# Kernel optimization log

Measured on AMD Instinct MI355X. Metric: run time of the kernel, lower is better.

The kernel has to match this reference:

```python
import jax, jax.numpy as jnp
import numpy as np

N, H = 8192, 256
TOP_K = 16          # k = min(top_k, N-1)
TEMPERATURE = 1.0
NEG_SLOPE = 0.2
NUM_SECTORS = 11


def setup_inputs() -> dict:
    key = jax.random.key(0)
    kE, kW, ka, ks, kA = jax.random.split(key, 5)
    embeddings = jax.random.normal(kE, (N, H), dtype=jnp.float32)
    # xavier-uniform-like scale for W (nn.Linear, bias=False)
    lim = float(np.sqrt(6.0 / (H + H)))
    W = jax.random.uniform(kW, (H, H), dtype=jnp.float32, minval=-lim, maxval=lim)
    # a ~ Normal(0, 1/sqrt(2H))
    a = jax.random.normal(ka, (2 * H,), dtype=jnp.float32) * (1.0 / np.sqrt(2 * H))
    sector_ids = jax.random.randint(ks, (N,), 0, NUM_SECTORS, dtype=jnp.int32)
    active_mask = jax.random.randint(kA, (N,), 0, 2, dtype=jnp.int32).astype(bool)
    return {"embeddings": embeddings, "W": W, "a": a,
            "sector_ids": sector_ids, "active_mask": active_mask}


def reference(embeddings, W, a, sector_ids, active_mask):
    # h = W(embeddings)  (torch Linear: x @ W.T)
    h = embeddings @ W.T                                   # [N, H]
    # attention[i,j] = leaky_relu(a . [h_i, h_j]) = leaky_relu(a1.h_i + a2.h_j)
    # (decomposition of the concat+matmul; same math, avoids O(N^2*2H) tensor)
    a1, a2 = a[:H], a[H:]
    s_i = h @ a1                                           # [N]
    s_j = h @ a2                                           # [N]
    att = jax.nn.leaky_relu(s_i[:, None] + s_j[None, :], NEG_SLOPE) / TEMPERATURE
    # combined mask: active pairs AND same sector
    mask = (active_mask[:, None] & active_mask[None, :]) \
           & (sector_ids[:, None] == sector_ids[None, :])  # [N, N]
    att = jnp.where(mask, att, -jnp.inf)
    k = min(TOP_K, N - 1)
    topk_values, topk_indices = jax.lax.top_k(att, k)      # [N, k] each
    valid = jnp.isfinite(topk_values)                      # invalid = masked-out slots
    # dense padded representation of (edge_index, edge_weight):
    # src = topk_indices, dst = row index, weight = topk_values where valid
    edge_weight = jnp.where(valid, topk_values, 0.0)
    return edge_weight, topk_indices, valid
```

## Files before the change

kernel.cpp:

```cpp
#include <hip/hip_runtime.h>

#define N 8192
#define H 256
#define TOPK 16
#define NSEC 11
#define NEG_SLOPE 0.2
#define NB 256
#define NT 256
#define RPB (N / NB)
#define NSL 8
#define SLICE (N / NSL)
#define NWB 256
#define IDX_SENT 0x7fffffff

__device__ __forceinline__ bool better(double av, int ai, double bv, int bi) {
    return (av > bv) || (av == bv && ai < bi);
}

__global__ __launch_bounds__(NT) void compute_v_s(
    const float* __restrict__ E, const float* __restrict__ W,
    const float* __restrict__ a,
    float* __restrict__ s1f, double* __restrict__ s2g,
    int* __restrict__ arrive)
{
    __shared__ float sa[2 * H];
    __shared__ double sv1[H];
    __shared__ double sv2[H];

    int t = threadIdx.x;
    int blk = blockIdx.x;
    int lane = t & 63;
    int w = t >> 6;

    if (blk == 0 && t <= NSEC) arrive[t] = 0;

    sa[t] = a[t];
    sa[t + H] = a[t + H];
    __syncthreads();

    {
        double a1_0 = 0.0, a1_1 = 0.0, a1_2 = 0.0, a1_3 = 0.0;
        double a2_0 = 0.0, a2_1 = 0.0, a2_2 = 0.0, a2_3 = 0.0;
        for (int j = 0; j < H; j += 4) {
            double w0 = (double)W[(j + 0) * H + t];
            double w1 = (double)W[(j + 1) * H + t];
            double w2 = (double)W[(j + 2) * H + t];
            double w3 = (double)W[(j + 3) * H + t];
            a1_0 += w0 * (double)sa[j + 0];
            a1_1 += w1 * (double)sa[j + 1];
            a1_2 += w2 * (double)sa[j + 2];
            a1_3 += w3 * (double)sa[j + 3];
            a2_0 += w0 * (double)sa[H + j + 0];
            a2_1 += w1 * (double)sa[H + j + 1];
            a2_2 += w2 * (double)sa[H + j + 2];
            a2_3 += w3 * (double)sa[H + j + 3];
        }
        sv1[t] = (a1_0 + a1_1) + (a1_2 + a1_3);
        sv2[t] = (a2_0 + a2_1) + (a2_2 + a2_3);
    }
    __syncthreads();

    {
        float4 e[RPB / 4];
#pragma unroll
        for (int q = 0; q < RPB / 4; ++q) {
            int row = blk * RPB + (w + 4 * q);
            e[q] = ((const float4*)(E + (size_t)row * H))[lane];
        }
        int base = lane * 4;
        double b10 = sv1[base + 0], b11 = sv1[base + 1],
               b12 = sv1[base + 2], b13 = sv1[base + 3];
        double b20 = sv2[base + 0], b21 = sv2[base + 1],
               b22 = sv2[base + 2], b23 = sv2[base + 3];
#pragma unroll
        for (int q = 0; q < RPB / 4; ++q) {
            int row = blk * RPB + (w + 4 * q);
            double acc1 = (double)e[q].x * b10 + (double)e[q].y * b11 +
                          (double)e[q].z * b12 + (double)e[q].w * b13;
            double acc2 = (double)e[q].x * b20 + (double)e[q].y * b21 +
                          (double)e[q].z * b22 + (double)e[q].w * b23;
            for (int o = 32; o > 0; o >>= 1) {
                acc1 += __shfl_down(acc1, o);
                acc2 += __shfl_down(acc2, o);
            }
            if (lane == 0) {
                s1f[row] = (float)acc1;
                s2g[row] = acc2;
            }
        }
    }
}

__global__ __launch_bounds__(NT) void slice_merge_write(
    const float* __restrict__ s1f, const double* __restrict__ s2g,
    const int* __restrict__ sec, const int* __restrict__ act,
    double* __restrict__ candV, int* __restrict__ candI,
    int* __restrict__ cnts, int* __restrict__ arrive,
    int* __restrict__ top_idx, int* __restrict__ fill_idx,
    int* __restrict__ m_arr, float* __restrict__ out)
{
    __shared__ double wV[4][TOPK];
    __shared__ int wI[4][TOPK];
    __shared__ int wCnt[4];
    __shared__ int sLast;

    int bx = blockIdx.x;
    int t = threadIdx.x;
    int lane = t & 63;
    int w = t >> 6;
    int* done = arrive + NSEC;

    if (bx < NSEC * NSL) {
        int c = bx >> 3;
        int sl = bx & 7;

        int j0 = sl * SLICE + 4 * t;
        int4 a4 = *(const int4*)(act + j0);
        int4 s4 = *(const int4*)(sec + j0);
        double2 d01 = *(const double2*)(s2g + j0);
        double2 d23 = *(const double2*)(s2g + j0 + 2);

        bool p0 = (a4.x != 0) && (s4.x == c);
        bool p1 = (a4.y != 0) && (s4.y == c);
        bool p2 = (a4.z != 0) && (s4.z == c);
        bool p3 = (a4.w != 0) && (s4.w == c);

        double v[4];
        int ix[4];
        v[0] = p0 ? d01.x : -INFINITY;  ix[0] = p0 ? (j0 + 0) : IDX_SENT;
        v[1] = p1 ? d01.y : -INFINITY;  ix[1] = p1 ? (j0 + 1) : IDX_SENT;
        v[2] = p2 ? d23.x : -INFINITY;  ix[2] = p2 ? (j0 + 2) : IDX_SENT;
        v[3] = p3 ? d23.y : -INFINITY;  ix[3] = p3 ? (j0 + 3) : IDX_SENT;

        int cnt = __popcll(__ballot(p0)) + __popcll(__ballot(p1)) +
                  __popcll(__ballot(p2)) + __popcll(__ballot(p3));

        for (int r = 0; r < TOPK; ++r) {
            double bv = v[0];
            int bi = ix[0];
#pragma unroll
            for (int p = 1; p < 4; ++p)
                if (better(v[p], ix[p], bv, bi)) { bv = v[p]; bi = ix[p]; }
            for (int o = 32; o > 0; o >>= 1) {
                double ov = __shfl_xor(bv, o);
                int oi = __shfl_xor(bi, o);
                if (better(ov, oi, bv, bi)) { bv = ov; bi = oi; }
            }
#pragma unroll
            for (int p = 0; p < 4; ++p)
                if (ix[p] == bi) { v[p] = -INFINITY; ix[p] = IDX_SENT; }
            if (lane == 0) {
                wV[w][r] = bv;
                wI[w][r] = bi;
            }
        }
        if (lane == 0) wCnt[w] = cnt;
        __syncthreads();

        if (w == 0) {
            double mv = wV[lane >> 4][lane & 15];
            int mi = wI[lane >> 4][lane & 15];
            for (int r = 0; r < TOPK; ++r) {
                double bv = mv;
                int bi = mi;
                for (int o = 32; o > 0; o >>= 1) {
                    double ov = __shfl_xor(bv, o);
                    int oi = __shfl_xor(bi, o);
                    if (better(ov, oi, bv, bi)) { bv = ov; bi = oi; }
                }
                if (mi == bi) { mv = -INFINITY; mi = IDX_SENT; }
                if (lane == 0) {
                    candV[bx * TOPK + r] = bv;
                    candI[bx * TOPK + r] = bi;
                }
            }
            if (lane == 0) {
                cnts[bx] = wCnt[0] + wCnt[1] + wCnt[2] + wCnt[3];
                __threadfence();
                int old = atomicAdd(&arrive[c], 1);
                sLast = (old == NSL - 1);
            }
        }
        __syncthreads();

        if (sLast) {
            __threadfence();

            if (w == 0) {
                const double* cbV = candV + (size_t)c * NSL * TOPK;
                const int* cbI = candI + (size_t)c * NSL * TOPK;
                double v0 = cbV[lane];
                int i0 = cbI[lane];
                double v1 = cbV[lane + 64];
                int i1 = cbI[lane + 64];
                for (int r = 0; r < TOPK; ++r) {
                    double bv;
                    int bi;
                    if (better(v0, i0, v1, i1)) { bv = v0; bi = i0; }
                    else                        { bv = v1; bi = i1; }
                    for (int o = 32; o > 0; o >>= 1) {
                        double ov = __shfl_xor(bv, o);
                        int oi = __shfl_xor(bi, o);
                        if (better(ov, oi, bv, bi)) { bv = ov; bi = oi; }
                    }
                    if (i0 == bi)      { v0 = -INFINITY; i0 = IDX_SENT; }
                    else if (i1 == bi) { v1 = -INFINITY; i1 = IDX_SENT; }
                    if (lane == 0) top_idx[c * TOPK + r] = (bi == IDX_SENT) ? -1 : bi;
                }
                int cl = (lane < NSL) ? cnts[c * NSL + lane] : 0;
                for (int o = 32; o > 0; o >>= 1) cl += __shfl_xor(cl, o);
                if (lane == 0) m_arr[c] = (cl < TOPK) ? cl : TOPK;
            } else if (w == 1) {
                int cnt2 = 0;
                for (int basej = 0; basej < N && cnt2 < TOPK; basej += 64) {
                    int j = basej + lane;
                    bool fail = !((act[j] != 0) && (sec[j] == c));
                    unsigned long long mask = __ballot(fail);
                    if (fail) {
                        int rank = cnt2 + __popcll(mask & ((1ull << lane) - 1));
                        if (rank < TOPK) fill_idx[c * TOPK + rank] = j;
                    }
                    cnt2 += __popcll(mask);
                }
            }
            __syncthreads();
            if (t == 0) {
                __threadfence();
                atomicAdd(done, 1);
            }
        }
    }

    if (t == 0) {
        while (__hip_atomic_load(done, __ATOMIC_RELAXED,
                                 __HIP_MEMORY_SCOPE_AGENT) < NSEC) {
            __builtin_amdgcn_s_sleep(8);
        }
    }
    __syncthreads();
    __threadfence();

    for (int gid = bx * NT + t; gid < N * TOPK; gid += NWB * NT) {
        int i = gid >> 4;
        int slot = gid & 15;

        float wgt = 0.0f;
        float fidx;
        float fvalid = 0.0f;

        if (act[i] == 0) {
            fidx = (float)slot;
        } else {
            int c = sec[i];
            int m = m_arr[c];
            if (slot < m) {
                int j = top_idx[c * TOPK + slot];
                double x = (double)s1f[i] + s2g[j];
                double attv = (x >= 0.0) ? x : NEG_SLOPE * x;
                wgt = (float)attv;
                fvalid = 1.0f;
                fidx = (float)j;
            } else {
                fidx = (float)fill_idx[c * TOPK + (slot - m)];
            }
        }

        out[gid] = wgt;
        out[N * TOPK + gid] = fidx;
        out[2 * N * TOPK + gid] = fvalid;
    }
}

extern "C" void kernel_launch(void* const* d_in, const int* in_sizes, int n_in,
                              void* d_out, int out_size, void* d_ws, size_t ws_size,
                              hipStream_t stream) {
    const float* E = (const float*)d_in[0];
    const float* W = (const float*)d_in[1];
    const float* a = (const float*)d_in[2];
    const int* sec = (const int*)d_in[3];
    const int* act = (const int*)d_in[4];

    char* ws = (char*)d_ws;
    double* s2g = (double*)ws;
    double* candV = s2g + N;
    float* s1f = (float*)(candV + NSEC * NSL * TOPK);
    int* candI = (int*)(s1f + N);
    int* cnts = candI + NSEC * NSL * TOPK;
    int* top_idx = cnts + NSEC * NSL;
    int* fill_idx = top_idx + NSEC * TOPK;
    int* m_arr = fill_idx + NSEC * TOPK;
    int* arrive = m_arr + NSEC;

    float* out = (float*)d_out;

    hipLaunchKernelGGL(compute_v_s, dim3(NB), dim3(NT), 0, stream,
                       E, W, a, s1f, s2g, arrive);
    hipLaunchKernelGGL(slice_merge_write, dim3(NWB), dim3(NT), 0, stream,
                       s1f, s2g, sec, act, candV, candI, cnts, arrive,
                       top_idx, fill_idx, m_arr, out);
}
```

Baseline: 132.6 us.

## Pad sync flags, replicate done flag, and prewrite inactive rows before spin-wait

The arrive counters and done flag are spread across separate 256-byte-strided slots. The last finishing sector now publishes eight replicated release flags, so the 256 waiting blocks poll different cache lines instead of one hot line. Each block also writes its inactive-row outputs before waiting, which overlaps part of the store traffic with the barrier. The output loop is unrolled to exactly two elements per thread, which hardcodes the grid geometry to NWB*NT*2 == N*TOPK.

Result: slower. 137.6 us (+3.7%).

```diff
diff --git a/kernel.cpp b/kernel.cpp
--- a/kernel.cpp
+++ b/kernel.cpp
@@ -13,6 +13,12 @@
 #define NWB 256
 #define IDX_SENT 0x7fffffff
 
+#define FSTRIDE 64
+#define ARR(c)  ((c) * FSTRIDE)
+#define DCNT    (NSEC * FSTRIDE)
+#define DREP(x) ((NSEC + 1 + (x)) * FSTRIDE)
+#define NFLAGS  ((NSEC + 1 + 8) * FSTRIDE)
+
 __device__ __forceinline__ bool better(double av, int ai, double bv, int bi) {
     return (av > bv) || (av == bv && ai < bi);
 }
@@ -21,7 +27,7 @@
     const float* __restrict__ E, const float* __restrict__ W,
     const float* __restrict__ a,
     float* __restrict__ s1f, double* __restrict__ s2g,
-    int* __restrict__ arrive)
+    int* __restrict__ flags)
 {
     __shared__ float sa[2 * H];
     __shared__ double sv1[H];
@@ -32,7 +38,9 @@
     int lane = t & 63;
     int w = t >> 6;
 
-    if (blk == 0 && t <= NSEC) arrive[t] = 0;
+    if (blk == 0) {
+        for (int z = t; z < NFLAGS; z += NT) flags[z] = 0;
+    }
 
     sa[t] = a[t];
     sa[t + H] = a[t + H];
@@ -95,7 +103,7 @@
     const float* __restrict__ s1f, const double* __restrict__ s2g,
     const int* __restrict__ sec, const int* __restrict__ act,
     double* __restrict__ candV, int* __restrict__ candI,
-    int* __restrict__ cnts, int* __restrict__ arrive,
+    int* __restrict__ cnts, int* __restrict__ flags,
     int* __restrict__ top_idx, int* __restrict__ fill_idx,
     int* __restrict__ m_arr, float* __restrict__ out)
 {
@@ -108,7 +116,6 @@
     int t = threadIdx.x;
     int lane = t & 63;
     int w = t >> 6;
-    int* done = arrive + NSEC;
 
     if (bx < NSEC * NSL) {
         int c = bx >> 3;
@@ -177,7 +184,7 @@
             if (lane == 0) {
                 cnts[bx] = wCnt[0] + wCnt[1] + wCnt[2] + wCnt[3];
                 __threadfence();
-                int old = atomicAdd(&arrive[c], 1);
+                int old = atomicAdd(&flags[ARR(c)], 1);
                 sLast = (old == NSL - 1);
             }
         }
@@ -226,48 +233,77 @@
             __syncthreads();
             if (t == 0) {
                 __threadfence();
-                atomicAdd(done, 1);
-            }
-        }
+                int od = atomicAdd(&flags[DCNT], 1);
+                if (od == NSEC - 1) {
+#pragma unroll
+                    for (int x = 0; x < 8; ++x)
+                        __hip_atomic_store(&flags[DREP(x)], 1,
+                                           __ATOMIC_RELEASE,
+                                           __HIP_MEMORY_SCOPE_AGENT);
+                }
+            }
+        }
+    }
+
+    int g0 = bx * (2 * NT) + t;
+    int g1 = g0 + NT;
+    int i0w = g0 >> 4, i1w = g1 >> 4;
+    int a0w = act[i0w], a1w = act[i1w];
+    int se0 = sec[i0w], se1 = sec[i1w];
+
+    if (a0w == 0) {
+        out[g0] = 0.0f;
+        out[N * TOPK + g0] = (float)(g0 & 15);
+        out[2 * N * TOPK + g0] = 0.0f;
+    }
+    if (a1w == 0) {
+        out[g1] = 0.0f;
+        out[N * TOPK + g1] = (float)(g1 & 15);
+        out[2 * N * TOPK + g1] = 0.0f;
     }
 
     if (t == 0) {
-        while (__hip_atomic_load(done, __ATOMIC_RELAXED,
-                                 __HIP_MEMORY_SCOPE_AGENT) < NSEC) {
-            __builtin_amdgcn_s_sleep(8);
+        while (__hip_atomic_load(&flags[DREP(bx & 7)], __ATOMIC_RELAXED,
+                                 __HIP_MEMORY_SCOPE_AGENT) == 0) {
+            __builtin_amdgcn_s_sleep(32);
         }
     }
     __syncthreads();
     __threadfence();
 
-    for (int gid = bx * NT + t; gid < N * TOPK; gid += NWB * NT) {
-        int i = gid >> 4;
-        int slot = gid & 15;
-
-        float wgt = 0.0f;
-        float fidx;
-        float fvalid = 0.0f;
-
-        if (act[i] == 0) {
-            fidx = (float)slot;
+    if (a0w != 0) {
+        int c = se0, m = m_arr[c], slot = g0 & 15;
+        float wgt = 0.0f, fvalid = 0.0f, fidx;
+        if (slot < m) {
+            int j = top_idx[c * TOPK + slot];
+            double x = (double)s1f[i0w] + s2g[j];
+            double attv = (x >= 0.0) ? x : NEG_SLOPE * x;
+            wgt = (float)attv;
+            fvalid = 1.0f;
+            fidx = (float)j;
         } else {
-            int c = sec[i];
-            int m = m_arr[c];
-            if (slot < m) {
-                int j = top_idx[c * TOPK + slot];
-                double x = (double)s1f[i] + s2g[j];
-                double attv = (x >= 0.0) ? x : NEG_SLOPE * x;
-                wgt = (float)attv;
-                fvalid = 1.0f;
-                fidx = (float)j;
-            } else {
-                fidx = (float)fill_idx[c * TOPK + (slot - m)];
-            }
-        }
-
-        out[gid] = wgt;
-        out[N * TOPK + gid] = fidx;
-        out[2 * N * TOPK + gid] = fvalid;
+            fidx = (float)fill_idx[c * TOPK + (slot - m)];
+        }
+        out[g0] = wgt;
+        out[N * TOPK + g0] = fidx;
+        out[2 * N * TOPK + g0] = fvalid;
+    }
+    if (a1w != 0) {
+        int c = se1, m = m_arr[c], slot = g1 & 15;
+        float wgt = 0.0f, fvalid = 0.0f, fidx;
+        if (slot < m) {
+            int j = top_idx[c * TOPK + slot];
+            double x = (double)s1f[i1w] + s2g[j];
+            double attv = (x >= 0.0) ? x : NEG_SLOPE * x;
+            wgt = (float)attv;
+            fvalid = 1.0f;
+            fidx = (float)j;
+        } else {
+            fidx = (float)fill_idx[c * TOPK + (slot - m)];
+        }
+        out[g1] = wgt;
+        out[N * TOPK + g1] = fidx;
+        out[2 * N * TOPK + g1] = fvalid;
     }
 }
 
@@ -289,13 +325,13 @@
     int* top_idx = cnts + NSEC * NSL;
     int* fill_idx = top_idx + NSEC * TOPK;
     int* m_arr = fill_idx + NSEC * TOPK;
-    int* arrive = m_arr + NSEC;
+    int* flags = (int*)((((size_t)(m_arr + NSEC)) + 255) & ~(size_t)255);
 
     float* out = (float*)d_out;
 
     hipLaunchKernelGGL(compute_v_s, dim3(NB), dim3(NT), 0, stream,
-                       E, W, a, s1f, s2g, arrive);
+                       E, W, a, s1f, s2g, flags);
     hipLaunchKernelGGL(slice_merge_write, dim3(NWB), dim3(NT), 0, stream,
-                       s1f, s2g, sec, act, candV, candI, cnts, arrive,
+                       s1f, s2g, sec, act, candV, candI, cnts, flags,
                        top_idx, fill_idx, m_arr, out);
 }
```
